# Performance work log

Hardware: AMD Instinct MI355X
Metric: run time of the kernel (lower is better)

## Reference

```python
import jax, jax.numpy as jnp
import numpy as np

FEATURE_COUNT = 41024
PAD_IDX = FEATURE_COUNT  # padding_idx in nn.Embedding
HIDDEN = 256
BATCH = 8192
BAG = 32


def setup_inputs() -> dict:
    key = jax.random.key(0)
    ks = jax.random.split(key, 9)
    emb = jax.random.normal(ks[0], (FEATURE_COUNT + 1, HIDDEN), jnp.float32) * 0.05
    emb = emb.at[PAD_IDX].set(0.0)  # padding row is zero, as in nn.Embedding(padding_idx=...)
    us = jax.random.randint(ks[1], (BATCH, BAG), 0, FEATURE_COUNT + 1)
    them = jax.random.randint(ks[2], (BATCH, BAG), 0, FEATURE_COUNT + 1)
    fc1_w = jax.random.normal(ks[3], (32, 2 * HIDDEN), jnp.float32) * 0.04
    fc1_b = jax.random.normal(ks[4], (32,), jnp.float32) * 0.01
    fc2_w = jax.random.normal(ks[5], (32, 32), jnp.float32) * 0.1
    fc2_b = jax.random.normal(ks[6], (32,), jnp.float32) * 0.01
    fc3_w = jax.random.normal(ks[7], (1, 32), jnp.float32) * 0.1
    fc3_b = jax.random.normal(ks[8], (1,), jnp.float32) * 0.01
    return {"us": us, "them": them, "emb": emb,
            "fc1_w": fc1_w, "fc1_b": fc1_b,
            "fc2_w": fc2_w, "fc2_b": fc2_b,
            "fc3_w": fc3_w, "fc3_b": fc3_b}


def _bag_sum(emb, idx):
    # gather [B, BAG, H], zero padded slots, sum over bag -> [B, H]
    e = emb[idx] * (idx != PAD_IDX)[..., None].astype(emb.dtype)
    return e.sum(axis=1)


def reference(us, them, emb, fc1_w, fc1_b, fc2_w, fc2_b, fc3_w, fc3_b):
    acc_us = _bag_sum(emb, us)      # [B, H]
    acc_them = _bag_sum(emb, them)  # [B, H]
    x = jnp.concatenate([acc_us, acc_them], axis=1)  # [B, 2H]
    x = jnp.clip(x @ fc1_w.T + fc1_b, 0.0, 1.0)
    x = jnp.clip(x @ fc2_w.T + fc2_b, 0.0, 1.0)
    return jnp.tanh(x @ fc3_w.T + fc3_b)  # [B, 1]
```

## Files before the change

### kernel.cpp

```cpp
#include <hip/hip_runtime.h>
#include <hip/hip_bf16.h>

constexpr int HIDDEN = 256;
constexpr int BAG    = 32;
constexpr int FEAT   = 41025;
constexpr int NJ     = 64;
constexpr int LDSS   = 264;

using bf16x8 = __attribute__((ext_vector_type(8))) short;
using f32x4  = __attribute__((ext_vector_type(4))) float;

__device__ inline unsigned short f2bf(float f) {
    union { float f; unsigned u; } x; x.f = f;
    return (unsigned short)((x.u + 0x7FFFu + ((x.u >> 16) & 1u)) >> 16);
}

__global__ __launch_bounds__(256, 2) void k0_project_mfma(
    const float* __restrict__ emb,
    const float* __restrict__ fc1_w,
    float*       __restrict__ P)
{
    __shared__ unsigned short a_lds[64 * LDSS];
    __shared__ unsigned short b_lds[64 * LDSS];

    const int tid = threadIdx.x;
    const int f0  = blockIdx.x * 64;
    const float4* emb4 = reinterpret_cast<const float4*>(emb);
    const float4* w4   = reinterpret_cast<const float4*>(fc1_w);

#pragma unroll
    for (int s = 0; s < 16; ++s) {
        const int idx4 = s * 256 + tid;
        const int row  = idx4 >> 6;
        const int kq4  = idx4 & 63;
        int grow = f0 + row; if (grow >= FEAT) grow = FEAT - 1;
        const float4 v = emb4[(size_t)grow * 64 + kq4];
        ushort4 b; b.x = f2bf(v.x); b.y = f2bf(v.y); b.z = f2bf(v.z); b.w = f2bf(v.w);
        *reinterpret_cast<ushort4*>(&a_lds[row * LDSS + kq4 * 4]) = b;
    }
#pragma unroll
    for (int s = 0; s < 16; ++s) {
        const int idx4 = s * 256 + tid;
        const int jr  = idx4 >> 7;
        const int kc4 = idx4 & 127;
        const int j   = jr + ((kc4 >= 64) ? 32 : 0);
        const int k4  = kc4 & 63;
        const float4 v = w4[idx4];
        ushort4 b; b.x = f2bf(v.x); b.y = f2bf(v.y); b.z = f2bf(v.z); b.w = f2bf(v.w);
        *reinterpret_cast<ushort4*>(&b_lds[j * LDSS + k4 * 4]) = b;
    }
    __syncthreads();

    const int lane = tid & 63, wave = tid >> 6;
    const int g = lane >> 4, ml = lane & 15;
    const int mw = wave * 16;

    f32x4 acc[4] = {{0.f,0.f,0.f,0.f},{0.f,0.f,0.f,0.f},
                    {0.f,0.f,0.f,0.f},{0.f,0.f,0.f,0.f}};
#pragma unroll
    for (int kt = 0; kt < 8; ++kt) {
        const bf16x8 af = *reinterpret_cast<const bf16x8*>(
            &a_lds[(mw + ml) * LDSS + kt * 32 + g * 8]);
#pragma unroll
        for (int nt = 0; nt < 4; ++nt) {
            const bf16x8 bf = *reinterpret_cast<const bf16x8*>(
                &b_lds[(nt * 16 + ml) * LDSS + kt * 32 + g * 8]);
            acc[nt] = __builtin_amdgcn_mfma_f32_16x16x32_bf16(af, bf, acc[nt], 0, 0, 0);
        }
    }

#pragma unroll
    for (int nt = 0; nt < 4; ++nt) {
#pragma unroll
        for (int r = 0; r < 4; ++r) {
            const int f = f0 + mw + g * 4 + r;
            if (f < FEAT)
                P[(size_t)f * NJ + nt * 16 + ml] = acc[nt][r];
        }
    }
}

__global__ __launch_bounds__(256) void k1_gather_mlp(
    const int*   __restrict__ us,
    const int*   __restrict__ them,
    const float* __restrict__ P,
    const float* __restrict__ b1,
    const float* __restrict__ w2, const float* __restrict__ b2,
    const float* __restrict__ w3, const float* __restrict__ b3,
    float*       __restrict__ out)
{
    __shared__ float w2_lds[32][33];
    __shared__ float y1_lds[4][32];

    const int tid  = threadIdx.x;
    const int wave = tid >> 6;
    const int lane = tid & 63;

    for (int k = tid; k < 32 * 32; k += 256)
        w2_lds[k >> 5][k & 31] = w2[k];
    __syncthreads();

    const int row = blockIdx.x * 4 + wave;
    int idx;
    {
        const int* up = us   + (size_t)row * BAG;
        const int* tp = them + (size_t)row * BAG;
        idx = (lane < BAG) ? up[lane] : tp[lane - BAG];
    }

    float acc = 0.f;
    const int srcbase = lane & 32;
#pragma unroll
    for (int i = 0; i < BAG; ++i) {
        const int f = __shfl(idx, srcbase + i);
        acc += P[(size_t)f * NJ + lane];
    }
    acc += __shfl_xor(acc, 32);

    if (lane < 32)
        y1_lds[wave][lane] = fminf(fmaxf(acc + b1[lane], 0.f), 1.f);
    __syncthreads();

    float r3 = 0.f;
    if (lane < 32) {
        float s = b2[lane];
#pragma unroll
        for (int k = 0; k < 32; ++k) s += y1_lds[wave][k] * w2_lds[lane][k];
        r3 = fminf(fmaxf(s, 0.f), 1.f) * w3[lane];
    }
    r3 += __shfl_xor(r3, 16); r3 += __shfl_xor(r3, 8); r3 += __shfl_xor(r3, 4);
    r3 += __shfl_xor(r3, 2);  r3 += __shfl_xor(r3, 1);
    if (lane == 0) out[row] = tanhf(r3 + b3[0]);
}

__global__ __launch_bounds__(256) void nnue_fused(
    const int*   __restrict__ us,
    const int*   __restrict__ them,
    const float* __restrict__ emb,
    const float* __restrict__ w1, const float* __restrict__ b1,
    const float* __restrict__ w2, const float* __restrict__ b2,
    const float* __restrict__ w3, const float* __restrict__ b3,
    float*       __restrict__ out)
{
    __shared__ float x_lds[4][2 * HIDDEN];
    __shared__ float y1_lds[4][32];
    __shared__ float y2_lds[4][32];

    const int tid  = threadIdx.x;
    const int wave = tid >> 6;
    const int lane = tid & 63;
    const int row  = blockIdx.x * 4 + wave;

    int myidx;
    {
        const int* up = us   + (size_t)row * BAG;
        const int* tp = them + (size_t)row * BAG;
        myidx = (lane < BAG) ? up[lane] : tp[lane - BAG];
    }
    const float4* emb4 = reinterpret_cast<const float4*>(emb);
    float4 accU = make_float4(0.f, 0.f, 0.f, 0.f);
    float4 accT = make_float4(0.f, 0.f, 0.f, 0.f);
#pragma unroll
    for (int i = 0; i < BAG; ++i) {
        const int iu = __shfl(myidx, i);
        const int it = __shfl(myidx, BAG + i);
        const float4 vu = emb4[(size_t)iu * (HIDDEN / 4) + lane];
        const float4 vt = emb4[(size_t)it * (HIDDEN / 4) + lane];
        accU.x += vu.x; accU.y += vu.y; accU.z += vu.z; accU.w += vu.w;
        accT.x += vt.x; accT.y += vt.y; accT.z += vt.z; accT.w += vt.w;
    }
    {
        float4* xv = reinterpret_cast<float4*>(&x_lds[wave][0]);
        xv[lane]      = accU;
        xv[64 + lane] = accT;
    }
    __syncthreads();
    {
        const int r    = tid >> 6;
        const int sub  = tid & 63;
        const int j    = sub >> 1;
        const int half = sub & 1;
        const float4* xr = reinterpret_cast<const float4*>(&x_lds[r][0]) + half * 64;
        const float4* wr = reinterpret_cast<const float4*>(w1 + (size_t)j * (2 * HIDDEN)) + half * 64;
        float s = 0.f;
#pragma unroll 8
        for (int k = 0; k < 64; ++k) {
            const float4 xk = xr[k];
            const float4 wk = wr[k];
            s += xk.x * wk.x + xk.y * wk.y + xk.z * wk.z + xk.w * wk.w;
        }
        s += __shfl_xor(s, 1);
        if (half == 0) { s += b1[j]; y1_lds[r][j] = fminf(fmaxf(s, 0.f), 1.f); }
    }
    __syncthreads();
    if (tid < 4 * 32) {
        const int r = tid >> 5;
        const int j = tid & 31;
        const float* wr = w2 + j * 32;
        float s = b2[j];
#pragma unroll
        for (int k = 0; k < 32; ++k) s += y1_lds[r][k] * wr[k];
        y2_lds[r][j] = fminf(fmaxf(s, 0.f), 1.f);
    }
    __syncthreads();
    if (tid < 4) {
        const int r = tid;
        float s = b3[0];
#pragma unroll
        for (int k = 0; k < 32; ++k) s += y2_lds[r][k] * w3[k];
        out[blockIdx.x * 4 + r] = tanhf(s);
    }
}

extern "C" void kernel_launch(void* const* d_in, const int* in_sizes, int n_in,
                              void* d_out, int out_size, void* d_ws, size_t ws_size,
                              hipStream_t stream) {
    const int*   us   = (const int*)  d_in[0];
    const int*   them = (const int*)  d_in[1];
    const float* emb  = (const float*)d_in[2];
    const float* w1   = (const float*)d_in[3];
    const float* b1   = (const float*)d_in[4];
    const float* w2   = (const float*)d_in[5];
    const float* b2   = (const float*)d_in[6];
    const float* w3   = (const float*)d_in[7];
    const float* b3   = (const float*)d_in[8];
    float* out = (float*)d_out;

    const int batch = in_sizes[0] / BAG;
    const size_t p_bytes = (size_t)FEAT * NJ * sizeof(float);

    if (ws_size >= p_bytes) {
        float* P = (float*)d_ws;
        const int grid0 = (FEAT + 63) / 64;
        k0_project_mfma<<<grid0, 256, 0, stream>>>(emb, w1, P);
        k1_gather_mlp<<<batch / 4, 256, 0, stream>>>(us, them, P,
                                                     b1, w2, b2, w3, b3, out);
    } else {
        nnue_fused<<<(batch + 3) / 4, 256, 0, stream>>>(us, them, emb,
                                                        w1, b1, w2, b2, w3, b3, out);
    }
}
```

Measured before the change: 28.93 us.

## Make projection kernel persistent with double-buffered async global-to-LDS loads

The embedding-projection kernel now runs as a persistent grid of 256 blocks that loop over 64-row tiles. Each block double-buffers the fp32 tiles in LDS using direct global-to-LDS loads with an XOR swizzle, and converts to bf16 at fragment-read time. The fc1 weight fragments are hoisted into registers once per block instead of being reloaded for every tile. The goal is to overlap the memory fetch with MFMA compute and remove per-tile weight reloading, at the cost of 128KB of LDS (one block per CU) and heavy register use.

```diff
diff --git a/kernel.cpp b/kernel.cpp
--- a/kernel.cpp
+++ b/kernel.cpp
@@ -5,78 +5,121 @@
 constexpr int BAG    = 32;
 constexpr int FEAT   = 41025;
 constexpr int NJ     = 64;
-constexpr int LDSS   = 264;
+constexpr int NTILES = (FEAT + 63) / 64;
+constexpr int GRID0  = 256;
 
 using bf16x8 = __attribute__((ext_vector_type(8))) short;
 using f32x4  = __attribute__((ext_vector_type(4))) float;
 
-__device__ inline unsigned short f2bf(float f) {
-    union { float f; unsigned u; } x; x.f = f;
-    return (unsigned short)((x.u + 0x7FFFu + ((x.u >> 16) & 1u)) >> 16);
-}
-
-__global__ __launch_bounds__(256, 2) void k0_project_mfma(
+typedef const __attribute__((address_space(1))) unsigned int* gas_u32;
+typedef __attribute__((address_space(3))) unsigned int*       las_u32;
+
+__device__ inline void load_lds16(const float* g, float* l) {
+    __builtin_amdgcn_global_load_lds((gas_u32)(const void*)g,
+                                     (las_u32)(void*)l, 16, 0, 0);
+}
+
+__device__ inline short f2bf(float f) {
+    __hip_bfloat16 h = __float2bfloat16(f);
+    return __builtin_bit_cast(short, h);
+}
+__device__ inline bf16x8 pack8(float4 a, float4 b) {
+    bf16x8 r;
+    r[0]=f2bf(a.x); r[1]=f2bf(a.y); r[2]=f2bf(a.z); r[3]=f2bf(a.w);
+    r[4]=f2bf(b.x); r[5]=f2bf(b.y); r[6]=f2bf(b.z); r[7]=f2bf(b.w);
+    return r;
+}
+
+__global__ __launch_bounds__(256) void k0_project_mfma(
     const float* __restrict__ emb,
     const float* __restrict__ fc1_w,
     float*       __restrict__ P)
 {
-    __shared__ unsigned short a_lds[64 * LDSS];
-    __shared__ unsigned short b_lds[64 * LDSS];
-
-    const int tid = threadIdx.x;
-    const int f0  = blockIdx.x * 64;
-    const float4* emb4 = reinterpret_cast<const float4*>(emb);
-    const float4* w4   = reinterpret_cast<const float4*>(fc1_w);
-
-#pragma unroll
-    for (int s = 0; s < 16; ++s) {
-        const int idx4 = s * 256 + tid;
-        const int row  = idx4 >> 6;
-        const int kq4  = idx4 & 63;
-        int grow = f0 + row; if (grow >= FEAT) grow = FEAT - 1;
-        const float4 v = emb4[(size_t)grow * 64 + kq4];
-        ushort4 b; b.x = f2bf(v.x); b.y = f2bf(v.y); b.z = f2bf(v.z); b.w = f2bf(v.w);
-        *reinterpret_cast<ushort4*>(&a_lds[row * LDSS + kq4 * 4]) = b;
-    }
-#pragma unroll
-    for (int s = 0; s < 16; ++s) {
-        const int idx4 = s * 256 + tid;
-        const int jr  = idx4 >> 7;
-        const int kc4 = idx4 & 127;
-        const int j   = jr + ((kc4 >= 64) ? 32 : 0);
-        const int k4  = kc4 & 63;
-        const float4 v = w4[idx4];
-        ushort4 b; b.x = f2bf(v.x); b.y = f2bf(v.y); b.z = f2bf(v.z); b.w = f2bf(v.w);
-        *reinterpret_cast<ushort4*>(&b_lds[j * LDSS + k4 * 4]) = b;
-    }
-    __syncthreads();
-
+    __shared__ float abuf[2][64 * 256];
+
+    const int tid  = threadIdx.x;
     const int lane = tid & 63, wave = tid >> 6;
     const int g = lane >> 4, ml = lane & 15;
     const int mw = wave * 16;
 
-    f32x4 acc[4] = {{0.f,0.f,0.f,0.f},{0.f,0.f,0.f,0.f},
-                    {0.f,0.f,0.f,0.f},{0.f,0.f,0.f,0.f}};
-#pragma unroll
-    for (int kt = 0; kt < 8; ++kt) {
-        const bf16x8 af = *reinterpret_cast<const bf16x8*>(
-            &a_lds[(mw + ml) * LDSS + kt * 32 + g * 8]);
+#pragma unroll
+    for (int i = 0; i < 16; ++i) {
+        const int j = mw + i;
+        const float* gp = fc1_w + (size_t)(j & 31) * 512 + ((j >> 5) << 8)
+                                + ((lane ^ (j & 7)) << 2);
+        load_lds16(gp, &abuf[1][j * 256]);
+    }
+    int t = blockIdx.x;
+    {
+#pragma unroll
+        for (int i = 0; i < 16; ++i) {
+            const int r = mw + i;
+            int grow = t * 64 + r; if (grow >= FEAT) grow = FEAT - 1;
+            const float* gp = emb + (size_t)grow * 256 + ((lane ^ (r & 7)) << 2);
+            load_lds16(gp, &abuf[0][r * 256]);
+        }
+    }
+    __syncthreads();
+
+    bf16x8 breg[4][8];
+#pragma unroll
+    for (int nt = 0; nt < 4; ++nt) {
+        const int rb = nt * 16 + ml, sw = rb & 7;
+        const float* rp = &abuf[1][rb * 256];
+#pragma unroll
+        for (int kt = 0; kt < 8; ++kt) {
+            const int q0 = kt * 8 + g * 2;
+            const float4 x0 = *reinterpret_cast<const float4*>(rp + ((q0 ^ sw) << 2));
+            const float4 x1 = *reinterpret_cast<const float4*>(rp + (((q0 + 1) ^ sw) << 2));
+            breg[nt][kt] = pack8(x0, x1);
+        }
+    }
+    __syncthreads();
+
+    int cur = 0;
+    while (true) {
+        const int nxt = t + GRID0;
+        if (nxt < NTILES) {
+            float* dst = abuf[cur ^ 1];
+#pragma unroll
+            for (int i = 0; i < 16; ++i) {
+                const int r = mw + i;
+                int grow = nxt * 64 + r; if (grow >= FEAT) grow = FEAT - 1;
+                const float* gp = emb + (size_t)grow * 256 + ((lane ^ (r & 7)) << 2);
+                load_lds16(gp, &dst[r * 256]);
+            }
+        }
+
+        f32x4 acc[4] = {{0.f,0.f,0.f,0.f},{0.f,0.f,0.f,0.f},
+                        {0.f,0.f,0.f,0.f},{0.f,0.f,0.f,0.f}};
+        {
+            const int ra = mw + ml, sw = ra & 7;
+            const float* rp = &abuf[cur][ra * 256];
+#pragma unroll
+            for (int kt = 0; kt < 8; ++kt) {
+                const int q0 = kt * 8 + g * 2;
+                const float4 x0 = *reinterpret_cast<const float4*>(rp + ((q0 ^ sw) << 2));
+                const float4 x1 = *reinterpret_cast<const float4*>(rp + (((q0 + 1) ^ sw) << 2));
+                const bf16x8 af = pack8(x0, x1);
+#pragma unroll
+                for (int nt = 0; nt < 4; ++nt)
+                    acc[nt] = __builtin_amdgcn_mfma_f32_16x16x32_bf16(af, breg[nt][kt],
+                                                                      acc[nt], 0, 0, 0);
+            }
+        }
 #pragma unroll
         for (int nt = 0; nt < 4; ++nt) {
-            const bf16x8 bf = *reinterpret_cast<const bf16x8*>(
-                &b_lds[(nt * 16 + ml) * LDSS + kt * 32 + g * 8]);
-            acc[nt] = __builtin_amdgcn_mfma_f32_16x16x32_bf16(af, bf, acc[nt], 0, 0, 0);
-        }
-    }
-
-#pragma unroll
-    for (int nt = 0; nt < 4; ++nt) {
-#pragma unroll
-        for (int r = 0; r < 4; ++r) {
-            const int f = f0 + mw + g * 4 + r;
-            if (f < FEAT)
-                P[(size_t)f * NJ + nt * 16 + ml] = acc[nt][r];
-        }
+#pragma unroll
+            for (int r = 0; r < 4; ++r) {
+                const int f = t * 64 + mw + g * 4 + r;
+                if (f < FEAT)
+                    P[(size_t)f * NJ + nt * 16 + ml] = acc[nt][r];
+            }
+        }
+
+        if (nxt >= NTILES) break;
+        __syncthreads();
+        cur ^= 1; t = nxt;
     }
 }
 
@@ -231,8 +274,7 @@
 
     if (ws_size >= p_bytes) {
         float* P = (float*)d_ws;
-        const int grid0 = (FEAT + 63) / 64;
-        k0_project_mfma<<<grid0, 256, 0, stream>>>(emb, w1, P);
+        k0_project_mfma<<<GRID0, 256, 0, stream>>>(emb, w1, P);
         k1_gather_mlp<<<batch / 4, 256, 0, stream>>>(us, them, P,
                                                      b1, w2, b2, w3, b3, out);
     } else {
```

New measurement: 28.70 us. About the same (-0.8%).

## Store projected table in bf16 and load MFMA operands directly without LDS

Applied to the files above, without the earlier changes.

The projection kernel now reads embedding rows and fc1 weights straight from global memory into registers and packs them to bf16 for MFMA, removing the LDS staging and barrier. The projected table P is written as bf16 instead of fp32, which halves the bytes gathered per bag element in the second kernel and the bytes written by the first. The cost is extra rounding of the layer-1 partial sums before they are accumulated, plus repeated fc1 weight loads per wave that now hit cache rather than shared memory.

```diff
diff --git a/kernel.cpp b/kernel.cpp
--- a/kernel.cpp
+++ b/kernel.cpp
@@ -5,67 +5,60 @@
 constexpr int BAG    = 32;
 constexpr int FEAT   = 41025;
 constexpr int NJ     = 64;
-constexpr int LDSS   = 264;
+constexpr int NTILES = (FEAT + 63) / 64;
 
 using bf16x8 = __attribute__((ext_vector_type(8))) short;
 using f32x4  = __attribute__((ext_vector_type(4))) float;
 
-__device__ inline unsigned short f2bf(float f) {
-    union { float f; unsigned u; } x; x.f = f;
-    return (unsigned short)((x.u + 0x7FFFu + ((x.u >> 16) & 1u)) >> 16);
-}
-
-__global__ __launch_bounds__(256, 2) void k0_project_mfma(
-    const float* __restrict__ emb,
-    const float* __restrict__ fc1_w,
-    float*       __restrict__ P)
+__device__ inline short f2bf(float f) {
+    __hip_bfloat16 h = __float2bfloat16(f);
+    return __builtin_bit_cast(short, h);
+}
+__device__ inline bf16x8 pack8(float4 a, float4 b) {
+    bf16x8 r;
+    r[0]=f2bf(a.x); r[1]=f2bf(a.y); r[2]=f2bf(a.z); r[3]=f2bf(a.w);
+    r[4]=f2bf(b.x); r[5]=f2bf(b.y); r[6]=f2bf(b.z); r[7]=f2bf(b.w);
+    return r;
+}
+
+__global__ __launch_bounds__(256) void k0_project_mfma(
+    const float*    __restrict__ emb,
+    const float*    __restrict__ fc1_w,
+    unsigned short* __restrict__ P)
 {
-    __shared__ unsigned short a_lds[64 * LDSS];
-    __shared__ unsigned short b_lds[64 * LDSS];
-
-    const int tid = threadIdx.x;
-    const int f0  = blockIdx.x * 64;
-    const float4* emb4 = reinterpret_cast<const float4*>(emb);
-    const float4* w4   = reinterpret_cast<const float4*>(fc1_w);
-
-#pragma unroll
-    for (int s = 0; s < 16; ++s) {
-        const int idx4 = s * 256 + tid;
-        const int row  = idx4 >> 6;
-        const int kq4  = idx4 & 63;
-        int grow = f0 + row; if (grow >= FEAT) grow = FEAT - 1;
-        const float4 v = emb4[(size_t)grow * 64 + kq4];
-        ushort4 b; b.x = f2bf(v.x); b.y = f2bf(v.y); b.z = f2bf(v.z); b.w = f2bf(v.w);
-        *reinterpret_cast<ushort4*>(&a_lds[row * LDSS + kq4 * 4]) = b;
-    }
-#pragma unroll
-    for (int s = 0; s < 16; ++s) {
-        const int idx4 = s * 256 + tid;
-        const int jr  = idx4 >> 7;
-        const int kc4 = idx4 & 127;
-        const int j   = jr + ((kc4 >= 64) ? 32 : 0);
-        const int k4  = kc4 & 63;
-        const float4 v = w4[idx4];
-        ushort4 b; b.x = f2bf(v.x); b.y = f2bf(v.y); b.z = f2bf(v.z); b.w = f2bf(v.w);
-        *reinterpret_cast<ushort4*>(&b_lds[j * LDSS + k4 * 4]) = b;
-    }
-    __syncthreads();
-
+    const int tid  = threadIdx.x;
     const int lane = tid & 63, wave = tid >> 6;
     const int g = lane >> 4, ml = lane & 15;
-    const int mw = wave * 16;
+    const int rbase = blockIdx.x * 64 + wave * 16;
+
+    int fr = rbase + ml; if (fr >= FEAT) fr = FEAT - 1;
+    const float* ap = emb + (size_t)fr * 256 + g * 8;
+
+    float4 a0[8], a1[8];
+#pragma unroll
+    for (int kt = 0; kt < 8; ++kt) {
+        a0[kt] = *reinterpret_cast<const float4*>(ap + kt * 32);
+        a1[kt] = *reinterpret_cast<const float4*>(ap + kt * 32 + 4);
+    }
+
+    const float* bp[4];
+#pragma unroll
+    for (int nt = 0; nt < 4; ++nt) {
+        const int j = nt * 16 + ml;
+        bp[nt] = fc1_w + (size_t)(j & 31) * 512 + ((j >> 5) << 8) + g * 8;
+    }
 
     f32x4 acc[4] = {{0.f,0.f,0.f,0.f},{0.f,0.f,0.f,0.f},
                     {0.f,0.f,0.f,0.f},{0.f,0.f,0.f,0.f}};
 #pragma unroll
     for (int kt = 0; kt < 8; ++kt) {
-        const bf16x8 af = *reinterpret_cast<const bf16x8*>(
-            &a_lds[(mw + ml) * LDSS + kt * 32 + g * 8]);
+        const bf16x8 af = pack8(a0[kt], a1[kt]);
 #pragma unroll
         for (int nt = 0; nt < 4; ++nt) {
-            const bf16x8 bf = *reinterpret_cast<const bf16x8*>(
-                &b_lds[(nt * 16 + ml) * LDSS + kt * 32 + g * 8]);
-            acc[nt] = __builtin_amdgcn_mfma_f32_16x16x32_bf16(af, bf, acc[nt], 0, 0, 0);
+            const float4 b0 = *reinterpret_cast<const float4*>(bp[nt] + kt * 32);
+            const float4 b1 = *reinterpret_cast<const float4*>(bp[nt] + kt * 32 + 4);
+            acc[nt] = __builtin_amdgcn_mfma_f32_16x16x32_bf16(af, pack8(b0, b1),
+                                                              acc[nt], 0, 0, 0);
         }
     }
 
@@ -73,17 +66,18 @@
     for (int nt = 0; nt < 4; ++nt) {
 #pragma unroll
         for (int r = 0; r < 4; ++r) {
-            const int f = f0 + mw + g * 4 + r;
+            const int f = rbase + g * 4 + r;
             if (f < FEAT)
-                P[(size_t)f * NJ + nt * 16 + ml] = acc[nt][r];
+                P[(size_t)f * NJ + nt * 16 + ml] =
+                    (unsigned short)f2bf(acc[nt][r]);
         }
     }
 }
 
 __global__ __launch_bounds__(256) void k1_gather_mlp(
-    const int*   __restrict__ us,
-    const int*   __restrict__ them,
-    const float* __restrict__ P,
+    const int*            __restrict__ us,
+    const int*            __restrict__ them,
+    const unsigned short* __restrict__ P,
     const float* __restrict__ b1,
     const float* __restrict__ w2, const float* __restrict__ b2,
     const float* __restrict__ w3, const float* __restrict__ b3,
@@ -113,7 +107,8 @@
 #pragma unroll
     for (int i = 0; i < BAG; ++i) {
         const int f = __shfl(idx, srcbase + i);
-        acc += P[(size_t)f * NJ + lane];
+        const unsigned short pv = P[(size_t)f * NJ + lane];
+        acc += __builtin_bit_cast(float, (unsigned)pv << 16);
     }
     acc += __shfl_xor(acc, 32);
 
@@ -227,12 +222,11 @@
     float* out = (float*)d_out;
 
     const int batch = in_sizes[0] / BAG;
-    const size_t p_bytes = (size_t)FEAT * NJ * sizeof(float);
+    const size_t p_bytes = (size_t)FEAT * NJ * sizeof(unsigned short);
 
     if (ws_size >= p_bytes) {
-        float* P = (float*)d_ws;
-        const int grid0 = (FEAT + 63) / 64;
-        k0_project_mfma<<<grid0, 256, 0, stream>>>(emb, w1, P);
+        unsigned short* P = (unsigned short*)d_ws;
+        k0_project_mfma<<<NTILES, 256, 0, stream>>>(emb, w1, P);
         k1_gather_mlp<<<batch / 4, 256, 0, stream>>>(us, them, P,
                                                      b1, w2, b2, w3, b3, out);
     } else {
```

Result: slower. 43.24 us (+49.5%).
